# Kernel optimization log

Measured on AMD Instinct MI355X. Metric: run time of the kernel, lower is better.

## Reference

```python
import jax, jax.numpy as jnp
import numpy as np

B, N, E, H, D = 64, 500, 128, 8, 16  # batch, pomo==graph size, embed, heads, qkv_dim
NEG = -1e9
LOGIT_CLIP = 10.0


def setup_inputs() -> dict:
    key = jax.random.key(0)
    ks = jax.random.split(key, 10)
    enc_nodes = jax.random.normal(ks[0], (B, N, E), dtype=jnp.float32)
    enc_first = jax.random.normal(ks[1], (B, N, E), dtype=jnp.float32)
    enc_last = jax.random.normal(ks[2], (B, N, E), dtype=jnp.float32)
    mask_bits = jax.random.uniform(ks[3], (B, N, N)) < 0.2
    ninf_mask = jnp.where(mask_bits, jnp.float32(NEG), jnp.float32(0.0))
    # Linear weights (torch layout [out_features, in_features])
    sc = 1.0 / np.sqrt(E)
    Wq_first = jax.random.normal(ks[4], (H * D, E), dtype=jnp.float32) * sc
    Wq_last = jax.random.normal(ks[5], (H * D, E), dtype=jnp.float32) * sc
    Wk = jax.random.normal(ks[6], (H * D, E), dtype=jnp.float32) * sc
    Wv = jax.random.normal(ks[7], (H * D, E), dtype=jnp.float32) * sc
    Wc = jax.random.normal(ks[8], (E, H * D), dtype=jnp.float32) / np.sqrt(H * D)
    bc = jax.random.normal(ks[9], (E,), dtype=jnp.float32) * 0.01
    return {"encoded_nodes": enc_nodes, "encoded_first_node": enc_first,
            "encoded_last_node": enc_last, "ninf_mask": ninf_mask,
            "Wq_first": Wq_first, "Wq_last": Wq_last, "Wk": Wk, "Wv": Wv,
            "Wc": Wc, "bc": bc}


def _heads(x, W):
    # x: [B, n, E], W: [H*D, E] -> [B, H, n, D]
    y = jnp.einsum('bne,fe->bnf', x, W)
    return y.reshape(x.shape[0], x.shape[1], H, D).transpose(0, 2, 1, 3)


def reference(encoded_nodes, encoded_first_node, encoded_last_node, ninf_mask,
              Wq_first, Wq_last, Wk, Wv, Wc, bc):
    # set_q1 + Wq_last projection, summed per POMO decoder
    q = _heads(encoded_first_node, Wq_first) + _heads(encoded_last_node, Wq_last)  # [B,H,N,D]
    k = _heads(encoded_nodes, Wk)  # [B,H,N,D]
    v = _heads(encoded_nodes, Wv)  # [B,H,N,D]
    # masked multi-head attention
    score = jnp.einsum('bhnd,bhgd->bhng', q, k) / jnp.sqrt(jnp.float32(D))
    score = score + ninf_mask[:, None, :, :]
    w = jax.nn.softmax(score, axis=-1)
    out = jnp.einsum('bhng,bhgd->bhnd', w, v)  # [B,H,N,D]
    out_concat = out.transpose(0, 2, 1, 3).reshape(B, N, H * D)
    mh = jnp.einsum('bnf,ef->bne', out_concat, Wc) + bc  # multi_head_combine
    # single-head pointer attention with tanh clipping
    s = jnp.einsum('bne,bge->bng', mh, encoded_nodes) / jnp.sqrt(jnp.float32(E))
    s = LOGIT_CLIP * jnp.tanh(s) + ninf_mask
    probs = jax.nn.softmax(s, axis=2)
    return probs
```

## Files before the change

kernel.cpp:

```cpp
#include <hip/hip_runtime.h>


#define B_ 64
#define N_ 500

typedef short bf16x8 __attribute__((ext_vector_type(8)));
typedef float f32x16 __attribute__((ext_vector_type(16)));
typedef unsigned short ushort8 __attribute__((ext_vector_type(8)));
typedef unsigned uint2v __attribute__((ext_vector_type(2)));

__device__ __forceinline__ float4 ld4(const float* p) { return *reinterpret_cast<const float4*>(p); }
__device__ __forceinline__ void st4(float* p, const float4 v) { *reinterpret_cast<float4*>(p) = v; }

__device__ __forceinline__ float fast_tanh(float x) {
    const float e = __expf(2.f * x);
    return 1.f - 2.f / (e + 1.f);
}
__device__ __forceinline__ unsigned short f2bf_rn(float x) {
    unsigned u = __float_as_uint(x);
    return (unsigned short)((u + 0x7FFFu + ((u >> 16) & 1u)) >> 16);
}
__device__ __forceinline__ float bf2f(unsigned short h) {
    return __uint_as_float(((unsigned)h) << 16);
}
__device__ __forceinline__ unsigned cvt_pk_bf16(float lo, float hi) {
    unsigned r;
    asm("v_cvt_pk_bf16_f32 %0, %1, %2" : "=v"(r) : "v"(lo), "v"(hi));
    return r;
}

__global__ __launch_bounds__(256) void mask_pack(
    const float* __restrict__ mask, unsigned long long* __restrict__ bits)
{
    const int w = threadIdx.x >> 6, l = threadIdx.x & 63;
    const int n = blockIdx.x * 4 + w;
    const int b = blockIdx.y;
    const float* mrow = &mask[((size_t)b * N_ + n) * N_];
    unsigned long long* brow = &bits[((size_t)b * N_ + n) * 8];
#pragma unroll
    for (int c = 0; c < 8; ++c) {
        const int j = c * 64 + l;
        const bool pred = (j >= N_) || (mrow[min(j, N_ - 1)] < -1.f);
        const unsigned long long bal = __ballot(pred);
        if (l == 0) brow[c] = bal;
    }
}

__global__ __launch_bounds__(256) void gemm_mfma(
    const float* __restrict__ A1, const float* __restrict__ W1a, const float* __restrict__ W1b,
    const float* __restrict__ A2, const float* __restrict__ W2a, const float* __restrict__ W2b,
    const float* __restrict__ bias, float* __restrict__ C, const int F, const int nterm)
{
    __shared__ unsigned short Ah[64 * 128];
    __shared__ unsigned short Al[64 * 128];
    __shared__ unsigned short Wh[64 * 128];
    __shared__ unsigned short Wl[64 * 128];

    const int t  = threadIdx.x;
    const int rb = blockIdx.y * 64;
    const int fb = blockIdx.x * 64;
    const int l  = t & 63;
    const int w  = t >> 6;
    const int half = l >> 5;
    const int mrow = 32 * (w >> 1) + (l & 31);
    const int ncol = 32 * (w & 1) + (l & 31);
    const int sr  = t >> 2;
    const int sc0 = (t & 3) * 32;

    f32x16 acc;
#pragma unroll
    for (int i = 0; i < 16; ++i) acc[i] = 0.f;

    for (int tt = 0; tt < nterm; ++tt) {
        const float* A  = tt ? A2 : A1;
        const float* Wa = tt ? W2a : W1a;
        const float* Wb = tt ? W2b : W1b;
        const float* W  = (fb < 128) ? Wa : Wb;
        const int frbase = fb & 127;

        if (tt) __syncthreads();

#pragma unroll
        for (int it = 0; it < 4; ++it) {
            const int c = sc0 + it * 8;
            const int chunk = c >> 3;
            const int dstA = sr * 128 + ((chunk ^ (sr & 7)) << 3);
            {
                const float4 v0 = ld4(&A[(size_t)(rb + sr) * 128 + c]);
                const float4 v1 = ld4(&A[(size_t)(rb + sr) * 128 + c + 4]);
                const float f[8] = {v0.x, v0.y, v0.z, v0.w, v1.x, v1.y, v1.z, v1.w};
                ushort8 hi, lo;
#pragma unroll
                for (int e = 0; e < 8; ++e) {
                    const unsigned short h = f2bf_rn(f[e]);
                    hi[e] = h;
                    lo[e] = f2bf_rn(f[e] - bf2f(h));
                }
                *reinterpret_cast<ushort8*>(&Ah[dstA]) = hi;
                *reinterpret_cast<ushort8*>(&Al[dstA]) = lo;
            }
            {
                const float4 v0 = ld4(&W[(size_t)(frbase + sr) * 128 + c]);
                const float4 v1 = ld4(&W[(size_t)(frbase + sr) * 128 + c + 4]);
                const float f[8] = {v0.x, v0.y, v0.z, v0.w, v1.x, v1.y, v1.z, v1.w};
                ushort8 hi, lo;
#pragma unroll
                for (int e = 0; e < 8; ++e) {
                    const unsigned short h = f2bf_rn(f[e]);
                    hi[e] = h;
                    lo[e] = f2bf_rn(f[e] - bf2f(h));
                }
                *reinterpret_cast<ushort8*>(&Wh[dstA]) = hi;
                *reinterpret_cast<ushort8*>(&Wl[dstA]) = lo;
            }
        }
        __syncthreads();

#pragma unroll
        for (int ks = 0; ks < 8; ++ks) {
            const int chA = (2 * ks + half) ^ (mrow & 7);
            const int chW = (2 * ks + half) ^ (ncol & 7);
            const bf16x8 ah = *reinterpret_cast<const bf16x8*>(&Ah[mrow * 128 + chA * 8]);
            const bf16x8 al = *reinterpret_cast<const bf16x8*>(&Al[mrow * 128 + chA * 8]);
            const bf16x8 wh = *reinterpret_cast<const bf16x8*>(&Wh[ncol * 128 + chW * 8]);
            const bf16x8 wl = *reinterpret_cast<const bf16x8*>(&Wl[ncol * 128 + chW * 8]);
            acc = __builtin_amdgcn_mfma_f32_32x32x16_bf16(ah, wh, acc, 0, 0, 0);
            acc = __builtin_amdgcn_mfma_f32_32x32x16_bf16(ah, wl, acc, 0, 0, 0);
            acc = __builtin_amdgcn_mfma_f32_32x32x16_bf16(al, wh, acc, 0, 0, 0);
        }
    }

    const int col = fb + ncol;
    const float bv = bias ? bias[col] : 0.f;
#pragma unroll
    for (int r = 0; r < 16; ++r) {
        const int row = rb + 32 * (w >> 1) + (r & 3) + 8 * (r >> 2) + 4 * half;
        C[(size_t)row * F + col] = acc[r] + bv;
    }
}

__global__ __launch_bounds__(256) void attn_mfma(
    const float* __restrict__ q, const float* __restrict__ kv,
    const unsigned* __restrict__ bits, float* __restrict__ att)
{
    __shared__ __align__(16) unsigned short Kh[32 * 16];
    __shared__ __align__(16) unsigned short Kl[32 * 16];
    __shared__ __align__(16) unsigned short Vh[32 * 40];
    __shared__ __align__(16) unsigned short Vl[32 * 40];
    __shared__ float Rinv[4][32];

    const int t  = threadIdx.x;
    const int w  = t >> 6;
    const int l  = t & 63;
    const int lr = l & 31;
    const int h  = l >> 5;
    const int rt = blockIdx.x;
    const int hh = blockIdx.y;
    const int b  = blockIdx.z;

    const int r_base = rt * 128 + w * 32;
    const int rc = min(r_base + lr, N_ - 1);

    bf16x8 qh, ql;
    {
        const float* qp = &q[((size_t)(b * N_ + rc)) * 128 + hh * 16 + 8 * h];
        const float4 a = ld4(qp), c = ld4(qp + 4);
        const float f[8] = {a.x, a.y, a.z, a.w, c.x, c.y, c.z, c.w};
#pragma unroll
        for (int e = 0; e < 8; ++e) {
            const float v = f[e] * 0.25f;
            const unsigned short hi = f2bf_rn(v);
            qh[e] = (short)hi;
            ql[e] = (short)f2bf_rn(v - bf2f(hi));
        }
    }

    const int sj   = t >> 3;
    const int sd   = (t & 7) * 2;
    const int kswz = sd ^ (8 * ((sj >> 2) & 1));
    const int vd   = t & 15;
    const int vj2  = (t >> 4) * 2;

    const f32x16 z = {0.f};
    f32x16 out;
#pragma unroll
    for (int i = 0; i < 16; ++i) out[i] = 0.f;
    float rowsum = 0.f;

    const unsigned* brow = &bits[(size_t)(b * N_ + rc) * 16];
    const int kchunk = h ^ ((lr >> 2) & 1);

    for (int js = 0; js < 16; ++js) {
        const int j0 = js * 32;
        __syncthreads();
        {
            const int jg = min(j0 + sj, N_ - 1);
            const float2 kk = *reinterpret_cast<const float2*>(
                &kv[((size_t)(b * N_ + jg)) * 256 + hh * 16 + sd]);
            const unsigned short h0 = f2bf_rn(kk.x), h1 = f2bf_rn(kk.y);
            const unsigned short l0 = f2bf_rn(kk.x - bf2f(h0)), l1 = f2bf_rn(kk.y - bf2f(h1));
            *reinterpret_cast<unsigned*>(&Kh[sj * 16 + kswz]) = (unsigned)h0 | ((unsigned)h1 << 16);
            *reinterpret_cast<unsigned*>(&Kl[sj * 16 + kswz]) = (unsigned)l0 | ((unsigned)l1 << 16);
        }
        {
            const int jg0 = min(j0 + vj2, N_ - 1), jg1 = min(j0 + vj2 + 1, N_ - 1);
            const float v0 = kv[((size_t)(b * N_ + jg0)) * 256 + 128 + hh * 16 + vd];
            const float v1 = kv[((size_t)(b * N_ + jg1)) * 256 + 128 + hh * 16 + vd];
            const unsigned short h0 = f2bf_rn(v0), h1 = f2bf_rn(v1);
            const unsigned short l0 = f2bf_rn(v0 - bf2f(h0)), l1 = f2bf_rn(v1 - bf2f(h1));
            *reinterpret_cast<unsigned*>(&Vh[vd * 40 + vj2]) = (unsigned)h0 | ((unsigned)h1 << 16);
            *reinterpret_cast<unsigned*>(&Vl[vd * 40 + vj2]) = (unsigned)l0 | ((unsigned)l1 << 16);
        }
        __syncthreads();

        const bf16x8 kfh = *reinterpret_cast<const bf16x8*>(&Kh[lr * 16 + kchunk * 8]);
        const bf16x8 kfl = *reinterpret_cast<const bf16x8*>(&Kl[lr * 16 + kchunk * 8]);
        f32x16 st = __builtin_amdgcn_mfma_f32_32x32x16_bf16(kfh, qh, z, 0, 0, 0);
        st = __builtin_amdgcn_mfma_f32_32x32x16_bf16(kfh, ql, st, 0, 0, 0);
        st = __builtin_amdgcn_mfma_f32_32x32x16_bf16(kfl, qh, st, 0, 0, 0);

        const unsigned bw = brow[js];
        float p[16];
#pragma unroll
        for (int g = 0; g < 16; ++g) {
            const int crow = (g & 3) + 8 * (g >> 2) + 4 * h;
            const float e = __expf(st[g]);
            p[g] = ((bw >> crow) & 1u) ? 0.f : e;
            rowsum += p[g];
        }

        unsigned wH[8], wL[8];
#pragma unroll
        for (int i = 0; i < 8; ++i) {
            wH[i] = cvt_pk_bf16(p[2 * i], p[2 * i + 1]);
            const float r0 = p[2 * i]     - __uint_as_float(wH[i] << 16);
            const float r1 = p[2 * i + 1] - __uint_as_float(wH[i] & 0xffff0000u);
            wL[i] = cvt_pk_bf16(r0, r1);
        }

        const uint2v aH0 = __builtin_amdgcn_permlane32_swap(wH[0], wH[2], false, false);
        const uint2v bH0 = __builtin_amdgcn_permlane32_swap(wH[1], wH[3], false, false);
        const uint2v aH1 = __builtin_amdgcn_permlane32_swap(wH[4], wH[6], false, false);
        const uint2v bH1 = __builtin_amdgcn_permlane32_swap(wH[5], wH[7], false, false);
        const uint2v aL0 = __builtin_amdgcn_permlane32_swap(wL[0], wL[2], false, false);
        const uint2v bL0 = __builtin_amdgcn_permlane32_swap(wL[1], wL[3], false, false);
        const uint2v aL1 = __builtin_amdgcn_permlane32_swap(wL[4], wL[6], false, false);
        const uint2v bL1 = __builtin_amdgcn_permlane32_swap(wL[5], wL[7], false, false);
        union { unsigned u[4]; bf16x8 v; } pH0 = {{aH0[0], bH0[0], aH0[1], bH0[1]}};
        union { unsigned u[4]; bf16x8 v; } pH1 = {{aH1[0], bH1[0], aH1[1], bH1[1]}};
        union { unsigned u[4]; bf16x8 v; } pL0 = {{aL0[0], bL0[0], aL0[1], bL0[1]}};
        union { unsigned u[4]; bf16x8 v; } pL1 = {{aL1[0], bL1[0], aL1[1], bL1[1]}};

        const bf16x8 vh0 = *reinterpret_cast<const bf16x8*>(&Vh[lr * 40 + 0 * 16 + 8 * h]);
        const bf16x8 vl0 = *reinterpret_cast<const bf16x8*>(&Vl[lr * 40 + 0 * 16 + 8 * h]);
        const bf16x8 vh1 = *reinterpret_cast<const bf16x8*>(&Vh[lr * 40 + 1 * 16 + 8 * h]);
        const bf16x8 vl1 = *reinterpret_cast<const bf16x8*>(&Vl[lr * 40 + 1 * 16 + 8 * h]);
        out = __builtin_amdgcn_mfma_f32_32x32x16_bf16(pH0.v, vh0, out, 0, 0, 0);
        out = __builtin_amdgcn_mfma_f32_32x32x16_bf16(pL0.v, vh0, out, 0, 0, 0);
        out = __builtin_amdgcn_mfma_f32_32x32x16_bf16(pH0.v, vl0, out, 0, 0, 0);
        out = __builtin_amdgcn_mfma_f32_32x32x16_bf16(pH1.v, vh1, out, 0, 0, 0);
        out = __builtin_amdgcn_mfma_f32_32x32x16_bf16(pL1.v, vh1, out, 0, 0, 0);
        out = __builtin_amdgcn_mfma_f32_32x32x16_bf16(pH1.v, vl1, out, 0, 0, 0);
    }

    rowsum += __shfl_xor(rowsum, 32, 64);
    if (h == 0) Rinv[w][lr] = 1.f / rowsum;
    const float4 i0 = *reinterpret_cast<const float4*>(&Rinv[w][4 * h]);
    const float4 i1 = *reinterpret_cast<const float4*>(&Rinv[w][8 + 4 * h]);
    const float4 i2 = *reinterpret_cast<const float4*>(&Rinv[w][16 + 4 * h]);
    const float4 i3 = *reinterpret_cast<const float4*>(&Rinv[w][24 + 4 * h]);
    const float iv[16] = {i0.x, i0.y, i0.z, i0.w, i1.x, i1.y, i1.z, i1.w,
                          i2.x, i2.y, i2.z, i2.w, i3.x, i3.y, i3.z, i3.w};
    if (lr < 16) {
#pragma unroll
        for (int g = 0; g < 16; ++g) {
            const int row = r_base + (g & 3) + 8 * (g >> 2) + 4 * h;
            if (row < N_)
                att[((size_t)(b * N_ + row)) * 128 + hh * 16 + lr] = out[g] * iv[g];
        }
    }
}

__global__ __launch_bounds__(256) void pointer_kernel(
    const float* __restrict__ mh, const float* __restrict__ enc,
    const float* __restrict__ mask, float* __restrict__ outp)
{
    __shared__ __align__(16) float Mt[16][68];
    __shared__ __align__(16) float Et[16][68];
    const int t = threadIdx.x;
    const int rt = blockIdx.x;
    const int b  = blockIdx.y;
    const int tj = t & 15;
    const int r0 = (t >> 4) * 4;
    const int g0 = tj * 4;
    const int srow = t >> 2;
    const int sde  = (t & 3) * 4;

    int rgl = rt * 64 + srow; if (rgl > 499) rgl = 499;
    float rs[4] = {0.f, 0.f, 0.f, 0.f};

    for (int gc = 0; gc < 8; ++gc) {
        float s[4][4];
#pragma unroll
        for (int i = 0; i < 4; ++i)
#pragma unroll
            for (int j = 0; j < 4; ++j) s[i][j] = 0.f;

        for (int ec = 0; ec < 8; ++ec) {
            __syncthreads();
            const float4 mv4 = ld4(&mh[((size_t)(b * N_ + rgl)) * 128 + ec * 16 + sde]);
            Mt[sde + 0][srow] = mv4.x; Mt[sde + 1][srow] = mv4.y;
            Mt[sde + 2][srow] = mv4.z; Mt[sde + 3][srow] = mv4.w;
            int gg = gc * 64 + srow; if (gg > 499) gg = 499;
            const float4 ev = ld4(&enc[((size_t)(b * N_ + gg)) * 128 + ec * 16 + sde]);
            Et[sde + 0][srow] = ev.x; Et[sde + 1][srow] = ev.y;
            Et[sde + 2][srow] = ev.z; Et[sde + 3][srow] = ev.w;
            __syncthreads();
#pragma unroll
            for (int d = 0; d < 16; ++d) {
                const float4 a4 = ld4(&Mt[d][r0]);
                const float4 e4 = ld4(&Et[d][g0]);
                const float a[4] = {a4.x, a4.y, a4.z, a4.w};
                const float e[4] = {e4.x, e4.y, e4.z, e4.w};
#pragma unroll
                for (int i = 0; i < 4; ++i)
#pragma unroll
                    for (int j = 0; j < 4; ++j) s[i][j] += a[i] * e[j];
            }
        }

#pragma unroll
        for (int i = 0; i < 4; ++i) {
            const int rg = rt * 64 + r0 + i;
            const int gg = gc * 64 + g0;
            const bool ok = (rg < 500) && (gg < 500);
            float4 mv;
            if (ok) mv = ld4(&mask[((size_t)b * N_ + rg) * N_ + gg]);
            else mv = make_float4(-1e9f, -1e9f, -1e9f, -1e9f);
            const float c = 0.08838834764831845f;
            float4 pv;
            pv.x = __expf(10.f * fast_tanh(s[i][0] * c) + mv.x);
            pv.y = __expf(10.f * fast_tanh(s[i][1] * c) + mv.y);
            pv.z = __expf(10.f * fast_tanh(s[i][2] * c) + mv.z);
            pv.w = __expf(10.f * fast_tanh(s[i][3] * c) + mv.w);
            rs[i] += pv.x + pv.y + pv.z + pv.w;
            if (ok) st4(&outp[((size_t)b * N_ + rg) * N_ + gg], pv);
        }
    }

#pragma unroll
    for (int m = 1; m < 16; m <<= 1)
#pragma unroll
        for (int i = 0; i < 4; ++i) rs[i] += __shfl_xor(rs[i], m, 64);

    float inv[4];
#pragma unroll
    for (int i = 0; i < 4; ++i) inv[i] = 1.f / rs[i];
    for (int gc = 0; gc < 8; ++gc) {
#pragma unroll
        for (int i = 0; i < 4; ++i) {
            const int rg = rt * 64 + r0 + i;
            const int gg = gc * 64 + g0;
            if (rg < 500 && gg < 500) {
                float* pp = &outp[((size_t)b * N_ + rg) * N_ + gg];
                float4 v = ld4(pp);
                v.x *= inv[i]; v.y *= inv[i]; v.z *= inv[i]; v.w *= inv[i];
                st4(pp, v);
            }
        }
    }
}

extern "C" void kernel_launch(void* const* d_in, const int* in_sizes, int n_in,
                              void* d_out, int out_size, void* d_ws, size_t ws_size,
                              hipStream_t stream) {
    const float* enc  = (const float*)d_in[0];
    const float* encf = (const float*)d_in[1];
    const float* encl = (const float*)d_in[2];
    const float* mask = (const float*)d_in[3];
    const float* Wqf  = (const float*)d_in[4];
    const float* Wql  = (const float*)d_in[5];
    const float* Wk   = (const float*)d_in[6];
    const float* Wv   = (const float*)d_in[7];
    const float* Wc   = (const float*)d_in[8];
    const float* bc   = (const float*)d_in[9];
    float* out = (float*)d_out;
    float* ws = (float*)d_ws;

    float* ws_q    = ws;
    float* ws_kv   = ws + 4096000;
    float* ws_att  = ws + 12288000;
    float* ws_mh   = ws_q;

    unsigned long long* bits64 = (unsigned long long*)d_out;

    mask_pack<<<dim3(125, 64), 256, 0, stream>>>(mask, bits64);
    gemm_mfma<<<dim3(2, 500), 256, 0, stream>>>(encf, Wqf, nullptr, encl, Wql, nullptr,
                                                nullptr, ws_q, 128, 2);
    gemm_mfma<<<dim3(4, 500), 256, 0, stream>>>(enc, Wk, Wv, nullptr, nullptr, nullptr,
                                                nullptr, ws_kv, 256, 1);
    attn_mfma<<<dim3(4, 8, 64), 256, 0, stream>>>(ws_q, ws_kv, (const unsigned*)d_out, ws_att);
    gemm_mfma<<<dim3(2, 500), 256, 0, stream>>>(ws_att, Wc, nullptr, nullptr, nullptr, nullptr,
                                                bc, ws_mh, 128, 1);
    pointer_kernel<<<dim3(8, 64), 256, 0, stream>>>(ws_mh, enc, mask, out);
}
```

Before: 434.2 us.

## Rewrite pointer kernel with split-bf16 MFMA and register-held probabilities

The pointer-attention kernel now computes mh·encᵀ with 32x32x16 bf16 MFMA, using a hi/lo bf16 split (three MFMAs) to keep close to fp32 accuracy, and stages operands in XOR-swizzled shared memory. Unnormalized probabilities for all 8 column passes stay in registers, so the output is written once after normalization instead of being written, read back and rewritten. This removes the scalar FMA loop and one full read-modify-write of the output. In exchange it adds bf16 split conversion work and high register pressure (128 floats for p). Mask loads become strided scalar reads in the MFMA layout.

```diff
diff --git a/kernel.cpp b/kernel.cpp
--- a/kernel.cpp
+++ b/kernel.cpp
@@ -281,92 +281,130 @@
     }
 }
 
-__global__ __launch_bounds__(256) void pointer_kernel(
+__global__ __launch_bounds__(256) void pointer_mfma(
     const float* __restrict__ mh, const float* __restrict__ enc,
     const float* __restrict__ mask, float* __restrict__ outp)
 {
-    __shared__ __align__(16) float Mt[16][68];
-    __shared__ __align__(16) float Et[16][68];
-    const int t = threadIdx.x;
+    __shared__ unsigned short Mh[64 * 128];
+    __shared__ unsigned short Ml[64 * 128];
+    __shared__ unsigned short Eh[64 * 128];
+    __shared__ unsigned short El[64 * 128];
+    __shared__ float Rpart[4][32];
+    __shared__ float RinvS[64];
+
+    const int t  = threadIdx.x;
     const int rt = blockIdx.x;
     const int b  = blockIdx.y;
-    const int tj = t & 15;
-    const int r0 = (t >> 4) * 4;
-    const int g0 = tj * 4;
-    const int srow = t >> 2;
-    const int sde  = (t & 3) * 4;
-
-    int rgl = rt * 64 + srow; if (rgl > 499) rgl = 499;
-    float rs[4] = {0.f, 0.f, 0.f, 0.f};
-
-    for (int gc = 0; gc < 8; ++gc) {
-        float s[4][4];
-#pragma unroll
-        for (int i = 0; i < 4; ++i)
-#pragma unroll
-            for (int j = 0; j < 4; ++j) s[i][j] = 0.f;
-
-        for (int ec = 0; ec < 8; ++ec) {
-            __syncthreads();
-            const float4 mv4 = ld4(&mh[((size_t)(b * N_ + rgl)) * 128 + ec * 16 + sde]);
-            Mt[sde + 0][srow] = mv4.x; Mt[sde + 1][srow] = mv4.y;
-            Mt[sde + 2][srow] = mv4.z; Mt[sde + 3][srow] = mv4.w;
-            int gg = gc * 64 + srow; if (gg > 499) gg = 499;
-            const float4 ev = ld4(&enc[((size_t)(b * N_ + gg)) * 128 + ec * 16 + sde]);
-            Et[sde + 0][srow] = ev.x; Et[sde + 1][srow] = ev.y;
-            Et[sde + 2][srow] = ev.z; Et[sde + 3][srow] = ev.w;
-            __syncthreads();
-#pragma unroll
-            for (int d = 0; d < 16; ++d) {
-                const float4 a4 = ld4(&Mt[d][r0]);
-                const float4 e4 = ld4(&Et[d][g0]);
-                const float a[4] = {a4.x, a4.y, a4.z, a4.w};
-                const float e[4] = {e4.x, e4.y, e4.z, e4.w};
-#pragma unroll
-                for (int i = 0; i < 4; ++i)
-#pragma unroll
-                    for (int j = 0; j < 4; ++j) s[i][j] += a[i] * e[j];
+    const int l  = t & 63;
+    const int w  = t >> 6;
+    const int half = l >> 5;
+    const int mrow = 32 * (w >> 1) + (l & 31);
+    const int ncol = 32 * (w & 1) + (l & 31);
+    const int sr  = t >> 2;
+    const int sc0 = (t & 3) * 32;
+    const int ch7 = l & 7;
+
+#pragma unroll
+    for (int it = 0; it < 4; ++it) {
+        const int c = sc0 + it * 8;
+        const int dst = sr * 128 + ((((c >> 3)) ^ (sr & 7)) << 3);
+        const float4 v0 = ld4(&mh[(size_t)(b * N_ + min(rt * 64 + sr, N_ - 1)) * 128 + c]);
+        const float4 v1 = ld4(&mh[(size_t)(b * N_ + min(rt * 64 + sr, N_ - 1)) * 128 + c + 4]);
+        const float f[8] = {v0.x, v0.y, v0.z, v0.w, v1.x, v1.y, v1.z, v1.w};
+        ushort8 hi, lo;
+#pragma unroll
+        for (int e = 0; e < 8; ++e) {
+            const unsigned short hv = f2bf_rn(f[e]);
+            hi[e] = hv;
+            lo[e] = f2bf_rn(f[e] - bf2f(hv));
+        }
+        *reinterpret_cast<ushort8*>(&Mh[dst]) = hi;
+        *reinterpret_cast<ushort8*>(&Ml[dst]) = lo;
+    }
+
+    f32x16 p[8];
+    f32x16 racc;
+#pragma unroll
+    for (int i = 0; i < 16; ++i) racc[i] = 0.f;
+
+    const float cinv = 0.08838834764831845f;
+
+#pragma unroll
+    for (int pass = 0; pass < 8; ++pass) {
+        __syncthreads();
+#pragma unroll
+        for (int it = 0; it < 4; ++it) {
+            const int c = sc0 + it * 8;
+            const int dst = sr * 128 + ((((c >> 3)) ^ (sr & 7)) << 3);
+            const int gg = min(pass * 64 + sr, N_ - 1);
+            const float4 v0 = ld4(&enc[(size_t)(b * N_ + gg) * 128 + c]);
+            const float4 v1 = ld4(&enc[(size_t)(b * N_ + gg) * 128 + c + 4]);
+            const float f[8] = {v0.x, v0.y, v0.z, v0.w, v1.x, v1.y, v1.z, v1.w};
+            ushort8 hi, lo;
+#pragma unroll
+            for (int e = 0; e < 8; ++e) {
+                const unsigned short hv = f2bf_rn(f[e]);
+                hi[e] = hv;
+                lo[e] = f2bf_rn(f[e] - bf2f(hv));
             }
-        }
-
-#pragma unroll
-        for (int i = 0; i < 4; ++i) {
-            const int rg = rt * 64 + r0 + i;
-            const int gg = gc * 64 + g0;
-            const bool ok = (rg < 500) && (gg < 500);
-            float4 mv;
-            if (ok) mv = ld4(&mask[((size_t)b * N_ + rg) * N_ + gg]);
-            else mv = make_float4(-1e9f, -1e9f, -1e9f, -1e9f);
-            const float c = 0.08838834764831845f;
-            float4 pv;
-            pv.x = __expf(10.f * fast_tanh(s[i][0] * c) + mv.x);
-            pv.y = __expf(10.f * fast_tanh(s[i][1] * c) + mv.y);
-            pv.z = __expf(10.f * fast_tanh(s[i][2] * c) + mv.z);
-            pv.w = __expf(10.f * fast_tanh(s[i][3] * c) + mv.w);
-            rs[i] += pv.x + pv.y + pv.z + pv.w;
-            if (ok) st4(&outp[((size_t)b * N_ + rg) * N_ + gg], pv);
-        }
-    }
-
-#pragma unroll
-    for (int m = 1; m < 16; m <<= 1)
-#pragma unroll
-        for (int i = 0; i < 4; ++i) rs[i] += __shfl_xor(rs[i], m, 64);
-
-    float inv[4];
-#pragma unroll
-    for (int i = 0; i < 4; ++i) inv[i] = 1.f / rs[i];
-    for (int gc = 0; gc < 8; ++gc) {
-#pragma unroll
-        for (int i = 0; i < 4; ++i) {
-            const int rg = rt * 64 + r0 + i;
-            const int gg = gc * 64 + g0;
-            if (rg < 500 && gg < 500) {
-                float* pp = &outp[((size_t)b * N_ + rg) * N_ + gg];
-                float4 v = ld4(pp);
-                v.x *= inv[i]; v.y *= inv[i]; v.z *= inv[i]; v.w *= inv[i];
-                st4(pp, v);
-            }
+            *reinterpret_cast<ushort8*>(&Eh[dst]) = hi;
+            *reinterpret_cast<ushort8*>(&El[dst]) = lo;
+        }
+        __syncthreads();
+
+        f32x16 acc;
+#pragma unroll
+        for (int i = 0; i < 16; ++i) acc[i] = 0.f;
+#pragma unroll
+        for (int ks = 0; ks < 8; ++ks) {
+            const int ch = (2 * ks + half) ^ ch7;
+            const bf16x8 ah = *reinterpret_cast<const bf16x8*>(&Mh[mrow * 128 + ch * 8]);
+            const bf16x8 al = *reinterpret_cast<const bf16x8*>(&Ml[mrow * 128 + ch * 8]);
+            const bf16x8 eh = *reinterpret_cast<const bf16x8*>(&Eh[ncol * 128 + ch * 8]);
+            const bf16x8 el = *reinterpret_cast<const bf16x8*>(&El[ncol * 128 + ch * 8]);
+            acc = __builtin_amdgcn_mfma_f32_32x32x16_bf16(ah, eh, acc, 0, 0, 0);
+            acc = __builtin_amdgcn_mfma_f32_32x32x16_bf16(ah, el, acc, 0, 0, 0);
+            acc = __builtin_amdgcn_mfma_f32_32x32x16_bf16(al, eh, acc, 0, 0, 0);
+        }
+
+        const int g = pass * 64 + ncol;
+#pragma unroll
+        for (int r = 0; r < 16; ++r) {
+            const int gr = rt * 64 + 32 * (w >> 1) + (r & 3) + 8 * (r >> 2) + 4 * half;
+            float mv = -1e9f;
+            if (gr < N_ && g < N_) mv = mask[((size_t)b * N_ + gr) * N_ + g];
+            const float pv = __expf(10.f * fast_tanh(acc[r] * cinv) + mv);
+            p[pass][r] = pv;
+            racc[r] += pv;
+        }
+    }
+
+#pragma unroll
+    for (int m = 1; m <= 16; m <<= 1)
+#pragma unroll
+        for (int r = 0; r < 16; ++r) racc[r] += __shfl_xor(racc[r], m, 64);
+
+    if ((l & 31) == 0) {
+#pragma unroll
+        for (int r = 0; r < 16; ++r)
+            Rpart[w][(r & 3) + 8 * (r >> 2) + 4 * half] = racc[r];
+    }
+    __syncthreads();
+    if (t < 64) {
+        const int hi = t >> 5, R = t & 31;
+        RinvS[t] = 1.f / (Rpart[2 * hi][R] + Rpart[2 * hi + 1][R]);
+    }
+    __syncthreads();
+
+#pragma unroll
+    for (int pass = 0; pass < 8; ++pass) {
+        const int g = pass * 64 + ncol;
+#pragma unroll
+        for (int r = 0; r < 16; ++r) {
+            const int br = 32 * (w >> 1) + (r & 3) + 8 * (r >> 2) + 4 * half;
+            const int gr = rt * 64 + br;
+            if (gr < N_ && g < N_)
+                outp[((size_t)b * N_ + gr) * N_ + g] = p[pass][r] * RinvS[br];
         }
     }
 }
@@ -402,5 +440,5 @@
     attn_mfma<<<dim3(4, 8, 64), 256, 0, stream>>>(ws_q, ws_kv, (const unsigned*)d_out, ws_att);
     gemm_mfma<<<dim3(2, 500), 256, 0, stream>>>(ws_att, Wc, nullptr, nullptr, nullptr, nullptr,
                                                 bc, ws_mh, 128, 1);
-    pointer_kernel<<<dim3(8, 64), 256, 0, stream>>>(ws_mh, enc, mask, out);
-}
+    pointer_mfma<<<dim3(8, 64), 256, 0, stream>>>(ws_mh, enc, mask, out);
+}
```

After: 435.9 us. Within noise of the previous version (+0.4%).
